# Performance work log

Measured on AMD Instinct MI355X. Metric: run time of the kernel, lower is better.

Reference implementation:

```python
import jax, jax.numpy as jnp
import numpy as np


def _conv(x, k):
    # x: (B,H,W,Cin), k: (kh,kw,Cin,Cout), SAME padding, stride 1
    return jax.lax.conv_general_dilated(
        x, k, window_strides=(1, 1), padding='SAME',
        dimension_numbers=('NHWC', 'HWIO', 'NHWC'))


def _hard_sigmoid(x):
    # Keras ConvLSTM2D default recurrent_activation='hard_sigmoid'
    return jnp.clip(0.2 * x + 0.5, 0.0, 1.0)


def _convlstm_layer(x_seq, k, rk, b):
    # x_seq: (B,T,H,W,Cin); gates packed i,f,c,o along channel axis (Keras order)
    B, T, H, W, _ = x_seq.shape
    F = rk.shape[2]
    h0 = jnp.zeros((B, H, W, F), x_seq.dtype)
    c0 = jnp.zeros((B, H, W, F), x_seq.dtype)

    def step(carry, xt):
        h, c = carry
        z = _conv(xt, k) + _conv(h, rk) + b
        i, f, g, o = jnp.split(z, 4, axis=-1)
        c_new = _hard_sigmoid(f) * c + _hard_sigmoid(i) * jnp.tanh(g)
        h_new = _hard_sigmoid(o) * jnp.tanh(c_new)
        return (h_new, c_new), h_new

    (h, c), ys = jax.lax.scan(step, (h0, c0), jnp.moveaxis(x_seq, 1, 0))
    return jnp.moveaxis(ys, 0, 1), h, c  # outputs (B,T,H,W,F), final h, c


def setup_inputs() -> dict:
    key = jax.random.key(0)
    ks = jax.random.split(key, 6)
    s = 0.05
    return {
        'x': jax.random.normal(ks[0], (8, 10, 64, 64, 1), jnp.float32),
        'k0': jax.random.normal(ks[1], (3, 3, 1, 256), jnp.float32) * s,
        'rk0': jax.random.normal(ks[2], (3, 3, 64, 256), jnp.float32) * s,
        'b0': jnp.zeros((256,), jnp.float32),
        'k1': jax.random.normal(ks[3], (3, 3, 64, 256), jnp.float32) * s,
        'rk1': jax.random.normal(ks[4], (3, 3, 64, 256), jnp.float32) * s,
        'b1': jnp.zeros((256,), jnp.float32),
    }


def reference(x, k0, rk0, b0, k1, rk1, b1):
    # layer 0
    seq0, h0, c0 = _convlstm_layer(x, k0, rk0, b0)
    # layer 1 consumes layer-0 sequence
    _, h1, c1 = _convlstm_layer(seq0, k1, rk1, b1)
    # states list [[h0,c0],[h1,c1]] -> stacked (layers=2, 2, B, H, W, F)
    return jnp.stack([jnp.stack([h0, c0]), jnp.stack([h1, c1])])
```

## Files before the change

### kernel.cpp

```cpp
#include <hip/hip_runtime.h>
#include <hip/hip_bf16.h>

typedef unsigned short u16;
typedef __attribute__((ext_vector_type(8))) short short8;
typedef __attribute__((ext_vector_type(4))) float f32x4;

#define T_STEPS 10
#define NB 8
#define HH 64
#define WW 64
#define FF 64
#define NGATE 256
#define HP 66
#define PIX (NB*HH*WW)

__device__ __forceinline__ u16 f2bf(float f) {
    unsigned u = __float_as_uint(f);
    u += 0x7FFF + ((u >> 16) & 1);
    return (u16)(u >> 16);
}
__device__ __forceinline__ float hsig(float x) {
    return fminf(fmaxf(0.2f * x + 0.5f, 0.0f), 1.0f);
}
__device__ __forceinline__ float ftanh(float x) {
    float e = __expf(2.0f * x);
    return 1.0f - 2.0f / (e + 1.0f);
}
__device__ __forceinline__ void gll16(const void* g, void* l) {
    __builtin_amdgcn_global_load_lds(
        (const __attribute__((address_space(1))) unsigned*)g,
        (__attribute__((address_space(3))) unsigned*)l, 16, 0, 0);
}

__global__ void wtrans_kernel(const float* __restrict__ W0,
                              const float* __restrict__ W1,
                              u16* __restrict__ BS, int K) {
    int total = (K >> 6) << 14;
    for (int o = blockIdx.x * blockDim.x + threadIdx.x; o < total;
         o += gridDim.x * blockDim.x) {
        int e = o & 7, lane = (o >> 3) & 63, g = (o >> 9) & 3;
        int ks = (o >> 11) & 1, fq = (o >> 12) & 3, kc = o >> 14;
        int quad = lane >> 4, l15 = lane & 15;
        int n = g * 64 + fq * 16 + l15;
        int k = kc * 64 + ks * 32 + quad * 8 + e;
        float v = (k < 576) ? W0[k * NGATE + n] : W1[(k - 576) * NGATE + n];
        BS[o] = f2bf(v);
    }
}

__device__ __forceinline__ void stageA(const u16* __restrict__ h0_prev,
                                       const u16* __restrict__ h1_prev,
                                       int kcs, int b, int y,
                                       int p0, int cb0, int p1, int cb1,
                                       u16* ldst0, u16* ldst1) {
    int tau = (kcs < 9) ? kcs : kcs - 9;
    const u16* src = (kcs < 9) ? h0_prev : h1_prev;
    int dy = tau / 3 - 1, dx = tau % 3 - 1;
    const u16* rbase = src + (((size_t)(b * HP + y + dy + 1)) * HP + dx + 1) * FF;
    gll16(rbase + (size_t)p0 * FF + cb0 * 8, ldst0);
    gll16(rbase + (size_t)p1 * FF + cb1 * 8, ldst1);
}

__global__ __launch_bounds__(256, 4)
void fused_step_kernel(const u16* __restrict__ h0_prev, u16* __restrict__ h0_new,
                       const u16* __restrict__ h1_prev, u16* __restrict__ h1_new,
                       const u16* __restrict__ B0S, const u16* __restrict__ B1S,
                       const float* __restrict__ x, const float* __restrict__ k0w,
                       const float* __restrict__ b0, const float* __restrict__ b1,
                       float* __restrict__ c0, float* __restrict__ c1,
                       float* __restrict__ oh0, float* __restrict__ oc0,
                       float* __restrict__ oh1, float* __restrict__ oc1,
                       int u) {
    int blk = blockIdx.x;
    int b = blk & 7;
    int k = blk >> 3;
    int role = (k >> 5) & 1;
    int y = (k & 31) | ((k >> 6) << 5);
    int pxb = b * 64 + y;
    if (role == 0 && u >= T_STEPS) return;
    if (role == 1 && u == 0) return;

    __shared__ __align__(16) u16 sA3[3][4096];
    __shared__ float xs[3][WW + 2];

    int tid = threadIdx.x;
    int lane = tid & 63, fq = tid >> 6;
    int quad = lane >> 4, l15 = lane & 15;

    const u16* BS = role ? B1S : B0S;
    int nch = role ? 18 : 9;

    if (role == 0 && tid < 3 * (WW + 2)) {
        int dyi = tid / (WW + 2), xx = tid - dyi * (WW + 2);
        int yy = y + dyi - 1, col = xx - 1;
        float v = 0.0f;
        if (yy >= 0 && yy < HH && col >= 0 && col < WW)
            v = x[(((size_t)b * T_STEPS + u) * HH + yy) * WW + col];
        xs[dyi][xx] = v;
    }

    int q0 = tid, q1 = 256 + tid;
    int p0 = q0 >> 3, cb0 = (q0 & 7) ^ (p0 & 7);
    int p1 = q1 >> 3, cb1 = (q1 & 7) ^ (p1 & 7);

    f32x4 acc[4][4];
#pragma unroll
    for (int mt = 0; mt < 4; ++mt)
#pragma unroll
        for (int g = 0; g < 4; ++g)
            acc[mt][g] = (f32x4){0.f, 0.f, 0.f, 0.f};

    stageA(h0_prev, h1_prev, 0, b, y, p0, cb0, p1, cb1,
           &sA3[0][(size_t)q0 * 8], &sA3[0][(size_t)q1 * 8]);
    asm volatile("s_waitcnt vmcnt(0) lgkmcnt(0)\n\ts_barrier" ::: "memory");
    if (nch > 1)
        stageA(h0_prev, h1_prev, 1, b, y, p0, cb0, p1, cb1,
               &sA3[1][(size_t)q0 * 8], &sA3[1][(size_t)q1 * 8]);

    int sx = l15 & 7;
    int cur = 0;
    for (int kc = 0; kc < nch; ++kc) {
#pragma unroll
        for (int ks = 0; ks < 2; ++ks) {
            short8 bF[4];
            const u16* bp = BS + (((size_t)kc << 14) | (fq << 12) | (ks << 11))
                          + lane * 8;
#pragma unroll
            for (int g = 0; g < 4; ++g)
                bF[g] = *(const short8*)(bp + ((size_t)g << 9));
            short8 aF[4];
#pragma unroll
            for (int mt = 0; mt < 4; ++mt) {
                int px = mt * 16 + l15;
                int chunk = px * 8 + ((ks * 4 + quad) ^ sx);
                aF[mt] = *(const short8*)&sA3[cur][(size_t)chunk * 8];
            }
#pragma unroll
            for (int mt = 0; mt < 4; ++mt)
#pragma unroll
                for (int g = 0; g < 4; ++g)
                    acc[mt][g] = __builtin_amdgcn_mfma_f32_16x16x32_bf16(
                        aF[mt], bF[g], acc[mt][g], 0, 0, 0);
        }
        {
            int ksrc = (kc + 2 < nch) ? kc + 2 : kc;
            int bdst = (cur + 2 >= 3) ? cur - 1 : cur + 2;
            stageA(h0_prev, h1_prev, ksrc, b, y, p0, cb0, p1, cb1,
                   &sA3[bdst][(size_t)q0 * 8], &sA3[bdst][(size_t)q1 * 8]);
        }
        asm volatile("s_waitcnt vmcnt(2) lgkmcnt(0)\n\ts_barrier" ::: "memory");
        cur = (cur == 2) ? 0 : cur + 1;
    }

    const float* bias = role ? b1 : b0;
    float* cbuf = role ? c1 : c0;
    u16* hout = role ? h1_new : h0_new;
    int wo = role ? (u == T_STEPS) : (u == T_STEPS - 1);
    float* outh = role ? oh1 : oh0;
    float* outc = role ? oc1 : oc0;

    int f = fq * 16 + l15;
    float bi = bias[f], bff = bias[64 + f], bg = bias[128 + f], bo = bias[192 + f];
    float wk[4][9];
    if (role == 0) {
#pragma unroll
        for (int g = 0; g < 4; ++g)
#pragma unroll
            for (int tau = 0; tau < 9; ++tau)
                wk[g][tau] = k0w[tau * NGATE + g * 64 + f];
    }
#pragma unroll
    for (int mt = 0; mt < 4; ++mt) {
#pragma unroll
        for (int r = 0; r < 4; ++r) {
            int xcol = mt * 16 + quad * 4 + r;
            size_t p = (size_t)pxb * 64 + xcol;
            float zi = acc[mt][0][r] + bi;
            float zf = acc[mt][1][r] + bff;
            float zg = acc[mt][2][r] + bg;
            float zo = acc[mt][3][r] + bo;
            if (role == 0) {
#pragma unroll
                for (int tau = 0; tau < 9; ++tau) {
                    float xv = xs[tau / 3][xcol + tau % 3];
                    zi += xv * wk[0][tau];
                    zf += xv * wk[1][tau];
                    zg += xv * wk[2][tau];
                    zo += xv * wk[3][tau];
                }
            }
            float cold = cbuf[p * FF + f];
            float cn = hsig(zf) * cold + hsig(zi) * ftanh(zg);
            float hn = hsig(zo) * ftanh(cn);
            cbuf[p * FF + f] = cn;
            hout[(((size_t)(b * HP + y + 1)) * HP + (xcol + 1)) * FF + f] = f2bf(hn);
            if (wo) { outh[p * FF + f] = hn; outc[p * FF + f] = cn; }
        }
    }
}

extern "C" void kernel_launch(void* const* d_in, const int* in_sizes, int n_in,
                              void* d_out, int out_size, void* d_ws, size_t ws_size,
                              hipStream_t stream) {
    const float* x   = (const float*)d_in[0];
    const float* k0  = (const float*)d_in[1];
    const float* rk0 = (const float*)d_in[2];
    const float* b0  = (const float*)d_in[3];
    const float* k1  = (const float*)d_in[4];
    const float* rk1 = (const float*)d_in[5];
    const float* b1  = (const float*)d_in[6];
    float* out = (float*)d_out;

    char* ws = (char*)d_ws;
    const size_t HPAD_BYTES = (size_t)NB * HP * HP * FF * 2;
    const size_t C_BYTES    = (size_t)PIX * FF * 4;

    u16* h0p[2]; u16* h1p[2];
    h0p[0] = (u16*)(ws);
    h0p[1] = (u16*)(ws + HPAD_BYTES);
    h1p[0] = (u16*)(ws + 2 * HPAD_BYTES);
    h1p[1] = (u16*)(ws + 3 * HPAD_BYTES);
    float* c0 = (float*)(ws + 4 * HPAD_BYTES);
    float* c1 = (float*)(ws + 4 * HPAD_BYTES + C_BYTES);
    u16* B0S  = (u16*)(ws + 4 * HPAD_BYTES + 2 * C_BYTES);
    u16* B1S  = (u16*)(ws + 4 * HPAD_BYTES + 2 * C_BYTES + (size_t)9 * 16384 * 2);

    hipMemsetAsync(ws, 0, 4 * HPAD_BYTES + 2 * C_BYTES, stream);

    wtrans_kernel<<<512, 256, 0, stream>>>(rk0, rk0, B0S, 576);
    wtrans_kernel<<<512, 256, 0, stream>>>(k1, rk1, B1S, 1152);

    float* oh0 = out;
    float* oc0 = out + (size_t)PIX * FF;
    float* oh1 = out + 2 * (size_t)PIX * FF;
    float* oc1 = out + 3 * (size_t)PIX * FF;

    for (int u = 0; u <= T_STEPS; ++u) {
        const u16* h0_prev = h0p[(u + 1) & 1];
        u16*       h0_new  = h0p[u & 1];
        const u16* h1_prev = h1p[u & 1];
        u16*       h1_new  = h1p[(u + 1) & 1];
        fused_step_kernel<<<1024, 256, 0, stream>>>(
            h0_prev, h0_new, h1_prev, h1_new, B0S, B1S,
            x, k0, b0, b1, c0, c1, oh0, oc0, oh1, oc1, u);
    }
}
```

Baseline: 481.5 us.

## Process two image rows per block to double M-tile and reuse B fragments

```diff
diff --git a/kernel.cpp b/kernel.cpp
--- a/kernel.cpp
+++ b/kernel.cpp
@@ -50,18 +50,24 @@
 
 __device__ __forceinline__ void stageA(const u16* __restrict__ h0_prev,
                                        const u16* __restrict__ h1_prev,
-                                       int kcs, int b, int y,
-                                       int p0, int cb0, int p1, int cb1,
-                                       u16* ldst0, u16* ldst1) {
+                                       int kcs, int b, int y0, int tid,
+                                       const int pxA[4], const int cbA[4],
+                                       u16* lbase) {
     int tau = (kcs < 9) ? kcs : kcs - 9;
     const u16* src = (kcs < 9) ? h0_prev : h1_prev;
     int dy = tau / 3 - 1, dx = tau % 3 - 1;
-    const u16* rbase = src + (((size_t)(b * HP + y + dy + 1)) * HP + dx + 1) * FF;
-    gll16(rbase + (size_t)p0 * FF + cb0 * 8, ldst0);
-    gll16(rbase + (size_t)p1 * FF + cb1 * 8, ldst1);
-}
-
-__global__ __launch_bounds__(256, 4)
+#pragma unroll
+    for (int i = 0; i < 4; ++i) {
+        int px = pxA[i];
+        int row = y0 + (px >> 6) + dy + 1;
+        int col = (px & 63) + dx + 1;
+        const u16* g = src + (((size_t)(b * HP + row)) * HP + col) * FF
+                     + cbA[i] * 8;
+        gll16(g, lbase + (size_t)(tid + i * 256) * 8);
+    }
+}
+
+__global__ __launch_bounds__(256, 2)
 void fused_step_kernel(const u16* __restrict__ h0_prev, u16* __restrict__ h0_new,
                        const u16* __restrict__ h1_prev, u16* __restrict__ h1_new,
                        const u16* __restrict__ B0S, const u16* __restrict__ B1S,
@@ -75,13 +81,12 @@
     int b = blk & 7;
     int k = blk >> 3;
     int role = (k >> 5) & 1;
-    int y = (k & 31) | ((k >> 6) << 5);
-    int pxb = b * 64 + y;
+    int y0 = (k & 31) * 2;
     if (role == 0 && u >= T_STEPS) return;
     if (role == 1 && u == 0) return;
 
-    __shared__ __align__(16) u16 sA3[3][4096];
-    __shared__ float xs[3][WW + 2];
+    __shared__ __align__(16) u16 sA3[3][8192];
+    __shared__ float xs[4][WW + 2];
 
     int tid = threadIdx.x;
     int lane = tid & 63, fq = tid >> 6;
@@ -90,32 +95,35 @@
     const u16* BS = role ? B1S : B0S;
     int nch = role ? 18 : 9;
 
-    if (role == 0 && tid < 3 * (WW + 2)) {
-        int dyi = tid / (WW + 2), xx = tid - dyi * (WW + 2);
-        int yy = y + dyi - 1, col = xx - 1;
-        float v = 0.0f;
-        if (yy >= 0 && yy < HH && col >= 0 && col < WW)
-            v = x[(((size_t)b * T_STEPS + u) * HH + yy) * WW + col];
-        xs[dyi][xx] = v;
-    }
-
-    int q0 = tid, q1 = 256 + tid;
-    int p0 = q0 >> 3, cb0 = (q0 & 7) ^ (p0 & 7);
-    int p1 = q1 >> 3, cb1 = (q1 & 7) ^ (p1 & 7);
-
-    f32x4 acc[4][4];
-#pragma unroll
-    for (int mt = 0; mt < 4; ++mt)
+    if (role == 0) {
+        for (int i = tid; i < 4 * (WW + 2); i += 256) {
+            int j = i / (WW + 2), xx = i - j * (WW + 2);
+            int yy = y0 + j - 1, col = xx - 1;
+            float v = 0.0f;
+            if (yy >= 0 && yy < HH && col >= 0 && col < WW)
+                v = x[(((size_t)b * T_STEPS + u) * HH + yy) * WW + col];
+            xs[j][xx] = v;
+        }
+    }
+
+    int pxA[4], cbA[4];
+#pragma unroll
+    for (int i = 0; i < 4; ++i) {
+        int q = tid + i * 256;
+        pxA[i] = q >> 3;
+        cbA[i] = (q & 7) ^ (pxA[i] & 7);
+    }
+
+    f32x4 acc[8][4];
+#pragma unroll
+    for (int mt = 0; mt < 8; ++mt)
 #pragma unroll
         for (int g = 0; g < 4; ++g)
             acc[mt][g] = (f32x4){0.f, 0.f, 0.f, 0.f};
 
-    stageA(h0_prev, h1_prev, 0, b, y, p0, cb0, p1, cb1,
-           &sA3[0][(size_t)q0 * 8], &sA3[0][(size_t)q1 * 8]);
+    stageA(h0_prev, h1_prev, 0, b, y0, tid, pxA, cbA, &sA3[0][0]);
     asm volatile("s_waitcnt vmcnt(0) lgkmcnt(0)\n\ts_barrier" ::: "memory");
-    if (nch > 1)
-        stageA(h0_prev, h1_prev, 1, b, y, p0, cb0, p1, cb1,
-               &sA3[1][(size_t)q0 * 8], &sA3[1][(size_t)q1 * 8]);
+    stageA(h0_prev, h1_prev, 1, b, y0, tid, pxA, cbA, &sA3[1][0]);
 
     int sx = l15 & 7;
     int cur = 0;
@@ -128,27 +136,23 @@
 #pragma unroll
             for (int g = 0; g < 4; ++g)
                 bF[g] = *(const short8*)(bp + ((size_t)g << 9));
-            short8 aF[4];
-#pragma unroll
-            for (int mt = 0; mt < 4; ++mt) {
+#pragma unroll
+            for (int mt = 0; mt < 8; ++mt) {
                 int px = mt * 16 + l15;
                 int chunk = px * 8 + ((ks * 4 + quad) ^ sx);
-                aF[mt] = *(const short8*)&sA3[cur][(size_t)chunk * 8];
-            }
-#pragma unroll
-            for (int mt = 0; mt < 4; ++mt)
+                short8 a = *(const short8*)&sA3[cur][(size_t)chunk * 8];
 #pragma unroll
                 for (int g = 0; g < 4; ++g)
                     acc[mt][g] = __builtin_amdgcn_mfma_f32_16x16x32_bf16(
-                        aF[mt], bF[g], acc[mt][g], 0, 0, 0);
+                        a, bF[g], acc[mt][g], 0, 0, 0);
+            }
         }
         {
             int ksrc = (kc + 2 < nch) ? kc + 2 : kc;
             int bdst = (cur + 2 >= 3) ? cur - 1 : cur + 2;
-            stageA(h0_prev, h1_prev, ksrc, b, y, p0, cb0, p1, cb1,
-                   &sA3[bdst][(size_t)q0 * 8], &sA3[bdst][(size_t)q1 * 8]);
-        }
-        asm volatile("s_waitcnt vmcnt(2) lgkmcnt(0)\n\ts_barrier" ::: "memory");
+            stageA(h0_prev, h1_prev, ksrc, b, y0, tid, pxA, cbA, &sA3[bdst][0]);
+        }
+        asm volatile("s_waitcnt vmcnt(4) lgkmcnt(0)\n\ts_barrier" ::: "memory");
         cur = (cur == 2) ? 0 : cur + 1;
     }
 
@@ -170,11 +174,12 @@
                 wk[g][tau] = k0w[tau * NGATE + g * 64 + f];
     }
 #pragma unroll
-    for (int mt = 0; mt < 4; ++mt) {
+    for (int mt = 0; mt < 8; ++mt) {
 #pragma unroll
         for (int r = 0; r < 4; ++r) {
-            int xcol = mt * 16 + quad * 4 + r;
-            size_t p = (size_t)pxb * 64 + xcol;
+            int pxl = mt * 16 + quad * 4 + r;
+            int rg = pxl >> 6, col = pxl & 63;
+            size_t p = ((size_t)(b * 64 + y0 + rg)) * 64 + col;
             float zi = acc[mt][0][r] + bi;
             float zf = acc[mt][1][r] + bff;
             float zg = acc[mt][2][r] + bg;
@@ -182,7 +187,7 @@
             if (role == 0) {
 #pragma unroll
                 for (int tau = 0; tau < 9; ++tau) {
-                    float xv = xs[tau / 3][xcol + tau % 3];
+                    float xv = xs[rg + tau / 3][col + tau % 3];
                     zi += xv * wk[0][tau];
                     zf += xv * wk[1][tau];
                     zg += xv * wk[2][tau];
@@ -193,7 +198,8 @@
             float cn = hsig(zf) * cold + hsig(zi) * ftanh(zg);
             float hn = hsig(zo) * ftanh(cn);
             cbuf[p * FF + f] = cn;
-            hout[(((size_t)(b * HP + y + 1)) * HP + (xcol + 1)) * FF + f] = f2bf(hn);
+            hout[(((size_t)(b * HP + y0 + rg + 1)) * HP + (col + 1)) * FF + f]
+                = f2bf(hn);
             if (wo) { outh[p * FF + f] = hn; outc[p * FF + f] = cn; }
         }
     }
@@ -240,7 +246,7 @@
         u16*       h0_new  = h0p[u & 1];
         const u16* h1_prev = h1p[u & 1];
         u16*       h1_new  = h1p[(u + 1) & 1];
-        fused_step_kernel<<<1024, 256, 0, stream>>>(
+        fused_step_kernel<<<512, 256, 0, stream>>>(
             h0_prev, h0_new, h1_prev, h1_new, B0S, B1S,
             x, k0, b0, b1, c0, c1, oh0, oc0, oh1, oc1, u);
     }
```

After: 563.9 us. 1.17x slower.

## Prefetch B weight fragments one chunk ahead with inline-asm double buffering

Applied to the files above, without the earlier changes.

```diff
diff --git a/kernel.cpp b/kernel.cpp
--- a/kernel.cpp
+++ b/kernel.cpp
@@ -61,7 +61,7 @@
     gll16(rbase + (size_t)p1 * FF + cb1 * 8, ldst1);
 }
 
-__global__ __launch_bounds__(256, 4)
+__global__ __launch_bounds__(256, 3)
 void fused_step_kernel(const u16* __restrict__ h0_prev, u16* __restrict__ h0_new,
                        const u16* __restrict__ h1_prev, u16* __restrict__ h1_new,
                        const u16* __restrict__ B0S, const u16* __restrict__ B1S,
@@ -110,47 +110,80 @@
         for (int g = 0; g < 4; ++g)
             acc[mt][g] = (f32x4){0.f, 0.f, 0.f, 0.f};
 
+    const u16* a0 = BS + (fq << 12) + lane * 8;
+    const u16* a1 = a0 + (1 << 11);
+    short8 bC[8], bN[8];
+
+#define BLOAD(B)                                                              \
+    asm volatile(                                                             \
+        "global_load_dwordx4 %0, %8, off\n\t"                                 \
+        "global_load_dwordx4 %1, %8, off offset:1024\n\t"                     \
+        "global_load_dwordx4 %2, %8, off offset:2048\n\t"                     \
+        "global_load_dwordx4 %3, %8, off offset:3072\n\t"                     \
+        "global_load_dwordx4 %4, %9, off\n\t"                                 \
+        "global_load_dwordx4 %5, %9, off offset:1024\n\t"                     \
+        "global_load_dwordx4 %6, %9, off offset:2048\n\t"                     \
+        "global_load_dwordx4 %7, %9, off offset:3072"                         \
+        : "=v"(B[0]), "=v"(B[1]), "=v"(B[2]), "=v"(B[3]),                     \
+          "=v"(B[4]), "=v"(B[5]), "=v"(B[6]), "=v"(B[7])                      \
+        : "v"(a0), "v"(a1))
+
+#define BWAIT(B)                                                              \
+    asm volatile("s_waitcnt vmcnt(10)"                                        \
+        : "+v"(B[0]), "+v"(B[1]), "+v"(B[2]), "+v"(B[3]),                     \
+          "+v"(B[4]), "+v"(B[5]), "+v"(B[6]), "+v"(B[7]))
+
     stageA(h0_prev, h1_prev, 0, b, y, p0, cb0, p1, cb1,
            &sA3[0][(size_t)q0 * 8], &sA3[0][(size_t)q1 * 8]);
-    asm volatile("s_waitcnt vmcnt(0) lgkmcnt(0)\n\ts_barrier" ::: "memory");
-    if (nch > 1)
-        stageA(h0_prev, h1_prev, 1, b, y, p0, cb0, p1, cb1,
-               &sA3[1][(size_t)q0 * 8], &sA3[1][(size_t)q1 * 8]);
+    BLOAD(bC);
+    asm volatile("s_waitcnt vmcnt(8) lgkmcnt(0)\n\ts_barrier" ::: "memory");
+    stageA(h0_prev, h1_prev, 1, b, y, p0, cb0, p1, cb1,
+           &sA3[1][(size_t)q0 * 8], &sA3[1][(size_t)q1 * 8]);
 
     int sx = l15 & 7;
     int cur = 0;
-    for (int kc = 0; kc < nch; ++kc) {
-#pragma unroll
-        for (int ks = 0; ks < 2; ++ks) {
-            short8 bF[4];
-            const u16* bp = BS + (((size_t)kc << 14) | (fq << 12) | (ks << 11))
-                          + lane * 8;
-#pragma unroll
-            for (int g = 0; g < 4; ++g)
-                bF[g] = *(const short8*)(bp + ((size_t)g << 9));
-            short8 aF[4];
-#pragma unroll
-            for (int mt = 0; mt < 4; ++mt) {
-                int px = mt * 16 + l15;
-                int chunk = px * 8 + ((ks * 4 + quad) ^ sx);
-                aF[mt] = *(const short8*)&sA3[cur][(size_t)chunk * 8];
-            }
-#pragma unroll
-            for (int mt = 0; mt < 4; ++mt)
-#pragma unroll
-                for (int g = 0; g < 4; ++g)
-                    acc[mt][g] = __builtin_amdgcn_mfma_f32_16x16x32_bf16(
-                        aF[mt], bF[g], acc[mt][g], 0, 0, 0);
-        }
-        {
-            int ksrc = (kc + 2 < nch) ? kc + 2 : kc;
-            int bdst = (cur + 2 >= 3) ? cur - 1 : cur + 2;
-            stageA(h0_prev, h1_prev, ksrc, b, y, p0, cb0, p1, cb1,
-                   &sA3[bdst][(size_t)q0 * 8], &sA3[bdst][(size_t)q1 * 8]);
-        }
-        asm volatile("s_waitcnt vmcnt(2) lgkmcnt(0)\n\ts_barrier" ::: "memory");
-        cur = (cur == 2) ? 0 : cur + 1;
-    }
+    int kc = 0;
+
+#define KBODY(BC_, BN_)                                                       \
+    {                                                                         \
+        int adv = (kc + 1 < nch) ? (1 << 14) : 0;     \
+        a0 += adv; a1 += adv;                                                 \
+        BLOAD(BN_);                                        \
+        BWAIT(BC_);                                       \
+        _Pragma("unroll")                                                     \
+        for (int ks = 0; ks < 2; ++ks) {                                      \
+            short8 aF[4];                                                     \
+            _Pragma("unroll")                                                 \
+            for (int mt = 0; mt < 4; ++mt) {                                  \
+                int px = mt * 16 + l15;                                       \
+                int chunk = px * 8 + ((ks * 4 + quad) ^ sx);                  \
+                aF[mt] = *(const short8*)&sA3[cur][(size_t)chunk * 8];        \
+            }                                                                 \
+            _Pragma("unroll")                                                 \
+            for (int mt = 0; mt < 4; ++mt)                                    \
+                _Pragma("unroll")                                             \
+                for (int g = 0; g < 4; ++g)                                   \
+                    acc[mt][g] = __builtin_amdgcn_mfma_f32_16x16x32_bf16(     \
+                        aF[mt], BC_[ks * 4 + g], acc[mt][g], 0, 0, 0);        \
+        }                                                                     \
+        {                                                                     \
+            int ksrc = (kc + 2 < nch) ? kc + 2 : kc;                          \
+            int bdst = (cur + 2 >= 3) ? cur - 1 : cur + 2;                    \
+            stageA(h0_prev, h1_prev, ksrc, b, y, p0, cb0, p1, cb1,            \
+                   &sA3[bdst][(size_t)q0 * 8], &sA3[bdst][(size_t)q1 * 8]);   \
+        }                                                                     \
+        asm volatile("s_waitcnt vmcnt(10) lgkmcnt(0)\n\ts_barrier" ::: "memory"); \
+        cur = (cur == 2) ? 0 : cur + 1;                                       \
+        ++kc;                                                                 \
+    }
+
+    while (kc < nch) {
+        KBODY(bC, bN);
+        if (kc < nch) KBODY(bN, bC);
+    }
+#undef KBODY
+#undef BLOAD
+#undef BWAIT
 
     const float* bias = role ? b1 : b0;
     float* cbuf = role ? c1 : c0;
```

After: 530.6 us. +10.2%, slower.
